# Kernel optimization log

Measured on AMD Instinct MI355X. Metric: run time of the kernel, lower is better.

Reference implementation:

```python
import jax, jax.numpy as jnp
import numpy as np

N_NODES = 20000
N_EDGES = 160000
N_GRAPHS = 16
NEG_INF = -1e30


def gcn_conv(x, edge_index, edge_weight, W, b):
    # PyG GCNConv with improved=True: add self-loops with weight 2.0,
    # symmetric degree normalization, linear transform, scatter-add aggregation.
    N = x.shape[0]
    row, col = edge_index[0], edge_index[1]
    loop = jnp.arange(N)
    row = jnp.concatenate([row, loop])
    col = jnp.concatenate([col, loop])
    ew = jnp.concatenate([edge_weight, jnp.full((N,), 2.0, edge_weight.dtype)])
    deg = jax.ops.segment_sum(ew, col, num_segments=N)
    dinv = jnp.where(deg > 0, deg ** -0.5, 0.0)  # deg_inv_sqrt, inf -> 0
    norm = dinv[row] * ew * dinv[col]            # [E+N]
    xl = x @ W                                   # [N, out]
    out = jax.ops.segment_sum(xl[row] * norm[:, None], col, num_segments=N)
    return out + b


def segment_softmax_masked(logits, mask, batch, num_segments):
    # softmax over masked entries, grouped by graph id (torch_geometric softmax
    # after masked_select); unmasked-out positions return 0.
    neg = jnp.asarray(NEG_INF, logits.dtype)
    ml = jnp.where(mask, logits, neg)
    mx = jax.ops.segment_max(ml, batch, num_segments=num_segments)
    ex = jnp.where(mask, jnp.exp(logits - mx[batch]), 0.0)
    s = jax.ops.segment_sum(ex, batch, num_segments=num_segments)
    return ex / jnp.maximum(s[batch], 1e-16)


def setup_inputs() -> dict:
    key = jax.random.key(0)
    ks = jax.random.split(key, 12)
    x = jax.random.normal(ks[0], (N_NODES, 5), dtype=jnp.float32)
    edge_index = jax.random.randint(ks[1], (2, N_EDGES), 0, N_NODES)
    edge_weight = jax.random.uniform(ks[2], (N_EDGES,), dtype=jnp.float32)
    mask = jax.random.randint(ks[3], (N_NODES,), 0, 2).astype(bool)
    batch = jnp.sort(jax.random.randint(ks[4], (N_NODES,), 0, N_GRAPHS))
    # parameters (Glorot-ish scaling)
    W1 = jax.random.normal(ks[5], (5, 1000), dtype=jnp.float32) / np.sqrt(5)
    b1 = jnp.zeros((1000,), jnp.float32)
    W2 = jax.random.normal(ks[6], (1000, 1000), dtype=jnp.float32) / np.sqrt(1000)
    b2 = jnp.zeros((1000,), jnp.float32)
    Wf = jax.random.normal(ks[7], (1000, 1), dtype=jnp.float32) / np.sqrt(1000)
    bf = jnp.zeros((1,), jnp.float32)
    return {"x": x, "edge_weight": edge_weight, "W1": W1, "b1": b1,
            "W2": W2, "b2": b2, "Wf": Wf, "bf": bf,
            "edge_index": edge_index, "mask": mask, "batch": batch}


def reference(x, edge_weight, W1, b1, W2, b2, Wf, bf, edge_index, mask, batch):
    h = jax.nn.relu(gcn_conv(x, edge_index, edge_weight, W1, b1))
    h = jax.nn.relu(gcn_conv(h, edge_index, edge_weight, W2, b2))
    # dropout treated as identity (eval mode) for a deterministic reference
    logits = (h @ Wf + bf)[:, 0]  # [N]
    return segment_softmax_masked(logits, mask, batch, N_GRAPHS)
```

## Files before the change

### kernel.cpp

```cpp
#include <hip/hip_runtime.h>

#define NN 20000
#define NE 160000
#define NG 16
#define KP 1024
#define MT2 160
#define MPAD2 (MT2*128)
#define NBLK 79

typedef __attribute__((ext_vector_type(8))) short bf16x8;
typedef __attribute__((ext_vector_type(4))) float f32x4;

#define GAS __attribute__((address_space(1)))
#define LAS __attribute__((address_space(3)))

__device__ __forceinline__ unsigned short f2bf(float f) {
    unsigned int u = __float_as_uint(f);
    u += 0x7FFFu + ((u >> 16) & 1u);
    return (unsigned short)(u >> 16);
}

__device__ __forceinline__ void gld_lds16(const char* g, char* l) {
    __builtin_amdgcn_global_load_lds((GAS void*)g, (LAS void*)l, 16, 0, 0);
}

__global__ void deg_cnt_kernel(const int* __restrict__ ei, const float* __restrict__ ew,
                               float* deg, int* cnt, const void* __restrict__ mask,
                               int* flags) {
    const int e = blockIdx.x * blockDim.x + threadIdx.x;
    if (e < 5000) {
        const unsigned v = ((const unsigned*)mask)[e];
        if (v > 1u) atomicOr(&flags[0], 1);
        if (v != 0u && v != 0x3F800000u) atomicOr(&flags[1], 1);
    }
    if (e >= NE) return;
    const int c = ei[NE + e];
    atomicAdd(&deg[c], ew[e]);
    atomicAdd(&cnt[c], 1);
}

__global__ __launch_bounds__(256) void partial_w2t_kernel(const int* __restrict__ cnt,
        const float* __restrict__ deg, const void* __restrict__ mask,
        const int* __restrict__ flags, int* __restrict__ mtmp,
        float* __restrict__ dinv, int* __restrict__ bcnt, int* __restrict__ bmsk,
        const float* __restrict__ W2, unsigned short* __restrict__ W2t) {
    const int bid = blockIdx.x;
    const int t = threadIdx.x;
    if (bid < NBLK) {
        const int i = bid * 256 + t;
        const int f0 = flags[0], f1 = flags[1];
        int c = 0, mv = 0;
        if (i < NN) {
            c = cnt[i];
            dinv[i] = 1.0f / sqrtf(2.0f + deg[i]);
            if (f0 == 0)      mv = ((const int*)mask)[i] != 0;
            else if (f1 == 0) mv = ((const unsigned*)mask)[i] != 0u;
            else              mv = ((const unsigned char*)mask)[i] != 0;
            mtmp[i] = mv;
        }
        __shared__ int sc[256], sm[256];
        sc[t] = c; sm[t] = mv;
        __syncthreads();
        for (int off = 128; off; off >>= 1) {
            if (t < off) { sc[t] += sc[t + off]; sm[t] += sm[t + off]; }
            __syncthreads();
        }
        if (t == 0) { bcnt[bid] = sc[0]; bmsk[bid] = sm[0]; }
    } else {
        __shared__ float tile[32][33];
        const int bw = bid - NBLK;
        const int n0 = (bw & 31) * 32;
        const int k0 = (bw >> 5) * 32;
        const int tx = t & 31, ty = t >> 5;
#pragma unroll
        for (int j = 0; j < 4; ++j) {
            const int k = k0 + ty + j * 8;
            const int n = n0 + tx;
            tile[ty + j * 8][tx] = (k < 1000 && n < 1000) ? W2[k * 1000 + n] : 0.0f;
        }
        __syncthreads();
#pragma unroll
        for (int j = 0; j < 4; ++j) {
            const int n = n0 + ty + j * 8;
            const int k = k0 + tx;
            W2t[(size_t)n * KP + k] = f2bf(tile[tx][ty + j * 8]);
        }
    }
}

__global__ __launch_bounds__(256) void apply_kernel(const int* __restrict__ cnt,
        const int* __restrict__ mtmp, const int* __restrict__ bcnt,
        const int* __restrict__ bmsk, const int* __restrict__ batch,
        int* __restrict__ offs, int* __restrict__ perm, int* __restrict__ bc,
        int* __restrict__ nm) {
    const int b = blockIdx.x, t = threadIdx.x;
    __shared__ int pbc[128], pbm[128];
    if (t < 128) {
        pbc[t] = (t < NBLK) ? bcnt[t] : 0;
        pbm[t] = (t < NBLK) ? bmsk[t] : 0;
    }
    __syncthreads();
    for (int off = 1; off < 128; off <<= 1) {
        int uc = 0, um = 0;
        if (t < 128 && t >= off) { uc = pbc[t - off]; um = pbm[t - off]; }
        __syncthreads();
        if (t < 128) { pbc[t] += uc; pbm[t] += um; }
        __syncthreads();
    }
    if (b == 0 && t == 0) nm[0] = pbm[NBLK - 1];
    const int bco = (b == 0) ? 0 : pbc[b - 1];
    const int bmo = (b == 0) ? 0 : pbm[b - 1];
    const int i = b * 256 + t;
    const int c  = (i < NN) ? cnt[i]  : 0;
    const int mv = (i < NN) ? mtmp[i] : 0;
    __shared__ int sc[256], sm[256];
    sc[t] = c; sm[t] = mv;
    __syncthreads();
    for (int off = 1; off < 256; off <<= 1) {
        const int uc = (t >= off) ? sc[t - off] : 0;
        const int um = (t >= off) ? sm[t - off] : 0;
        __syncthreads();
        sc[t] += uc; sm[t] += um;
        __syncthreads();
    }
    if (i < NN) {
        offs[i] = bco + sc[t] - c;
        if (mv) {
            const int pos = bmo + sm[t] - 1;
            perm[pos] = i;
            bc[pos] = batch[i];
        }
    }
}

__global__ void scatter_kernel(const int* __restrict__ ei, const float* __restrict__ ew,
                               const float* __restrict__ dinv, const int* __restrict__ offs,
                               int* cursor, int* __restrict__ ssrc, float* __restrict__ snorm) {
    const int e = blockIdx.x * blockDim.x + threadIdx.x;
    if (e >= NE) return;
    const int r = ei[e], c = ei[NE + e];
    const int pos = atomicAdd(&cursor[c], 1);
    const int idx = offs[c] + pos;
    ssrc[idx] = r;
    snorm[idx] = dinv[r] * ew[e] * dinv[c];
}

__global__ __launch_bounds__(256) void axf_kernel(const float* __restrict__ x,
        const int* __restrict__ ssrc, const float* __restrict__ snorm,
        const int* __restrict__ offs, const int* __restrict__ cnt,
        const float* __restrict__ dinv, float* __restrict__ Axf) {
    const int i = blockIdx.x * blockDim.x + threadIdx.x;
    if (i >= NN) return;
    float a0=0,a1=0,a2=0,a3=0,a4=0;
    const int s0 = offs[i], n = cnt[i];
    for (int e = s0; e < s0 + n; ++e) {
        const int r = ssrc[e];
        const float w = snorm[e];
        const float* xr = x + r * 5;
        a0 += w*xr[0]; a1 += w*xr[1]; a2 += w*xr[2]; a3 += w*xr[3]; a4 += w*xr[4];
    }
    const float wl = 2.0f * dinv[i] * dinv[i];
    const float* xi = x + i * 5;
    a0 += wl*xi[0]; a1 += wl*xi[1]; a2 += wl*xi[2]; a3 += wl*xi[3]; a4 += wl*xi[4];
    float* o = Axf + i * 5;
    o[0]=a0; o[1]=a1; o[2]=a2; o[3]=a3; o[4]=a4;
}

__global__ __launch_bounds__(256) void aggW1_kernel(const float* __restrict__ Axf,
        const float* __restrict__ W1, const float* __restrict__ b1,
        const int* __restrict__ ssrc, const float* __restrict__ snorm,
        const int* __restrict__ offs, const int* __restrict__ cnt,
        const float* __restrict__ dinv, const int* __restrict__ perm,
        const int* __restrict__ nm, unsigned short* __restrict__ G) {
    const int t = threadIdx.x;
    __shared__ int s_nm;
    if (t == 0) s_nm = nm[0];
    __syncthreads();
    const int nmv = s_nm;
    const int npad = (nmv + 127) & ~127;
    const int j0 = blockIdx.x * 8;
    if (j0 >= npad) return;

    const bool active = t < 250;
    const int c0 = active ? t * 4 : 1000 + (t - 250) * 4;
    float w[5][4];
    float bb[4];
    if (active) {
#pragma unroll
        for (int f = 0; f < 5; ++f) {
            const float4 wv = *(const float4*)(W1 + f * 1000 + c0);
            w[f][0] = wv.x; w[f][1] = wv.y; w[f][2] = wv.z; w[f][3] = wv.w;
        }
        const float4 b4 = *(const float4*)(b1 + c0);
        bb[0] = b4.x; bb[1] = b4.y; bb[2] = b4.z; bb[3] = b4.w;
    } else {
#pragma unroll
        for (int f = 0; f < 5; ++f) { w[f][0]=0; w[f][1]=0; w[f][2]=0; w[f][3]=0; }
        bb[0]=0; bb[1]=0; bb[2]=0; bb[3]=0;
    }

    __shared__ float4 sax4[64];
    __shared__ float2 sax2[64];
    for (int jj = 0; jj < 8; ++jj) {
        const int j = j0 + jj;
        if (j >= npad) break;
        float acc0 = 0.f, acc1 = 0.f, acc2 = 0.f, acc3 = 0.f;
        if (j < nmv) {
            const int i = perm[j];
            const int s0 = offs[i], n = cnt[i];
            const int total = n + 1;
            for (int base = 0; base < total; base += 64) {
                const int m = (total - base < 64) ? (total - base) : 64;
                __syncthreads();
                if (t < m) {
                    const int idx = base + t;
                    int r; float we;
                    if (idx < n) { r = ssrc[s0 + idx]; we = snorm[s0 + idx]; }
                    else         { r = i; const float dv = dinv[i]; we = 2.0f * dv * dv; }
                    const float* axr = Axf + r * 5;
                    sax4[t] = make_float4(axr[0], axr[1], axr[2], axr[3]);
                    sax2[t] = make_float2(axr[4], we);
                }
                __syncthreads();
#pragma unroll 2
                for (int e = 0; e < m; ++e) {
                    const float4 a4 = sax4[e];
                    const float2 a2 = sax2[e];
                    float z0 = bb[0], z1 = bb[1], z2 = bb[2], z3 = bb[3];
                    z0 += a4.x*w[0][0]; z1 += a4.x*w[0][1]; z2 += a4.x*w[0][2]; z3 += a4.x*w[0][3];
                    z0 += a4.y*w[1][0]; z1 += a4.y*w[1][1]; z2 += a4.y*w[1][2]; z3 += a4.y*w[1][3];
                    z0 += a4.z*w[2][0]; z1 += a4.z*w[2][1]; z2 += a4.z*w[2][2]; z3 += a4.z*w[2][3];
                    z0 += a4.w*w[3][0]; z1 += a4.w*w[3][1]; z2 += a4.w*w[3][2]; z3 += a4.w*w[3][3];
                    z0 += a2.x*w[4][0]; z1 += a2.x*w[4][1]; z2 += a2.x*w[4][2]; z3 += a2.x*w[4][3];
                    const float we = a2.y;
                    acc0 += we * fmaxf(z0, 0.f); acc1 += we * fmaxf(z1, 0.f);
                    acc2 += we * fmaxf(z2, 0.f); acc3 += we * fmaxf(z3, 0.f);
                }
            }
        }
        ushort4 pk;
        pk.x = f2bf(acc0); pk.y = f2bf(acc1); pk.z = f2bf(acc2); pk.w = f2bf(acc3);
        *(ushort4*)(G + (size_t)j * KP + c0) = pk;
    }
}

__global__ __launch_bounds__(256) void gemm_kernel(const unsigned short* __restrict__ A,
                                                   const unsigned short* __restrict__ B,
                                                   const float* __restrict__ b2,
                                                   const float* __restrict__ Wf,
                                                   const int* __restrict__ nm,
                                                   float* __restrict__ logitsC) {
    __shared__ unsigned short As[4096];
    __shared__ unsigned short Bs[4096];
    const int tid = threadIdx.x;
    __shared__ int s_nm;
    if (tid == 0) s_nm = nm[0];
    __syncthreads();
    const int nmv = s_nm;
    const int mstrips = (nmv + 127) >> 7;
    const int bid = blockIdx.x;
    const int tm = (bid >> 6) * 8 + (bid & 7);
    const int tn = (bid >> 3) & 7;
    if (tm >= mstrips) return;
    const int lane = tid & 63;
    const int wv = tid >> 6;
    const int wr = wv >> 1, wc = wv & 1;

    const int chunk = ((tid & 3) ^ ((tid >> 3) & 3)) * 16;
    const int rsub = tid >> 2;
    const char* Ag = (const char*)(A + (size_t)(tm * 128 + rsub) * KP) + chunk;
    const char* Bg = (const char*)(B + (size_t)(tn * 128 + rsub) * KP) + chunk;
    char* AsW = (char*)As + wv * 1024;
    char* BsW = (char*)Bs + wv * 1024;

    f32x4 acc[4][4];
#pragma unroll
    for (int i = 0; i < 4; ++i)
#pragma unroll
        for (int j = 0; j < 4; ++j) acc[i][j] = (f32x4){0.f, 0.f, 0.f, 0.f};

    const int m = lane & 15;
    const int quad = lane >> 4;
    const int sw = quad ^ ((m >> 1) & 3);
    const int aoff = (wr * 64 + m) * 64 + sw * 16;
    const int boff = (wc * 64 + m) * 64 + sw * 16;

    for (int kk = 0; kk < KP; kk += 32) {
        __syncthreads();
        const int kb = kk * 2;
        gld_lds16(Ag + kb,             AsW);
        gld_lds16(Ag + kb + 64 * 2048, AsW + 4096);
        gld_lds16(Bg + kb,             BsW);
        gld_lds16(Bg + kb + 64 * 2048, BsW + 4096);
        __syncthreads();
        bf16x8 af[4], bfv[4];
#pragma unroll
        for (int mt = 0; mt < 4; ++mt)
            af[mt] = *(const bf16x8*)((const char*)As + aoff + mt * 1024);
#pragma unroll
        for (int nt = 0; nt < 4; ++nt)
            bfv[nt] = *(const bf16x8*)((const char*)Bs + boff + nt * 1024);
#pragma unroll
        for (int mt = 0; mt < 4; ++mt)
#pragma unroll
            for (int nt = 0; nt < 4; ++nt)
                acc[mt][nt] = __builtin_amdgcn_mfma_f32_16x16x32_bf16(af[mt], bfv[nt], acc[mt][nt], 0, 0, 0);
    }

    const int col0 = tn * 128 + wc * 64 + m;
    const int row00 = tm * 128 + wr * 64 + quad * 4;
#pragma unroll
    for (int mt = 0; mt < 4; ++mt) {
        float ps0 = 0.f, ps1 = 0.f, ps2 = 0.f, ps3 = 0.f;
#pragma unroll
        for (int nt = 0; nt < 4; ++nt) {
            const int c = col0 + nt * 16;
            const float bbv = (c < 1000) ? b2[c] : 0.0f;
            const float wfv = (c < 1000) ? Wf[c] : 0.0f;
            ps0 += fmaxf(acc[mt][nt][0] + bbv, 0.f) * wfv;
            ps1 += fmaxf(acc[mt][nt][1] + bbv, 0.f) * wfv;
            ps2 += fmaxf(acc[mt][nt][2] + bbv, 0.f) * wfv;
            ps3 += fmaxf(acc[mt][nt][3] + bbv, 0.f) * wfv;
        }
#pragma unroll
        for (int msk = 1; msk < 16; msk <<= 1) {
            ps0 += __shfl_xor(ps0, msk);
            ps1 += __shfl_xor(ps1, msk);
            ps2 += __shfl_xor(ps2, msk);
            ps3 += __shfl_xor(ps3, msk);
        }
        if (m == 0) {
            const int row = row00 + mt * 16;
            if (row + 0 < nmv) atomicAdd(&logitsC[row + 0], ps0);
            if (row + 1 < nmv) atomicAdd(&logitsC[row + 1], ps1);
            if (row + 2 < nmv) atomicAdd(&logitsC[row + 2], ps2);
            if (row + 3 < nmv) atomicAdd(&logitsC[row + 3], ps3);
        }
    }
}

__global__ __launch_bounds__(256) void softmax_kernel(const float* __restrict__ logitsC,
        const int* __restrict__ perm, const int* __restrict__ bc,
        const int* __restrict__ nm, float* __restrict__ out) {
    const int g = blockIdx.x;
    const int t = threadIdx.x;
    __shared__ int s_lo, s_hi;
    __shared__ float red[4];
    __shared__ float sval;
    if (t == 0) {
        const int nmv = nm[0];
        int lo = 0, hi = nmv;
        while (lo < hi) { const int mid = (lo + hi) >> 1; if (bc[mid] < g) lo = mid + 1; else hi = mid; }
        s_lo = lo;
        int lo2 = lo, hi2 = nmv;
        while (lo2 < hi2) { const int mid = (lo2 + hi2) >> 1; if (bc[mid] < g + 1) lo2 = mid + 1; else hi2 = mid; }
        s_hi = lo2;
    }
    __syncthreads();
    const int lo = s_lo, hi = s_hi;
    float mx = -1e30f;
    for (int i = lo + t; i < hi; i += 256) mx = fmaxf(mx, logitsC[i]);
    for (int off = 32; off; off >>= 1) mx = fmaxf(mx, __shfl_down(mx, off));
    if ((t & 63) == 0) red[t >> 6] = mx;
    __syncthreads();
    if (t == 0) sval = fmaxf(fmaxf(red[0], red[1]), fmaxf(red[2], red[3]));
    __syncthreads();
    mx = sval;
    __syncthreads();
    float sm = 0.f;
    for (int i = lo + t; i < hi; i += 256) sm += expf(logitsC[i] - mx);
    for (int off = 32; off; off >>= 1) sm += __shfl_down(sm, off);
    if ((t & 63) == 0) red[t >> 6] = sm;
    __syncthreads();
    if (t == 0) sval = red[0] + red[1] + red[2] + red[3];
    __syncthreads();
    const float inv = 1.0f / fmaxf(sval, 1e-16f);
    for (int i = lo + t; i < hi; i += 256)
        out[perm[i]] = expf(logitsC[i] - mx) * inv;
}

extern "C" void kernel_launch(void* const* d_in, const int* in_sizes, int n_in,
                              void* d_out, int out_size, void* d_ws, size_t ws_size,
                              hipStream_t stream) {
    (void)in_sizes; (void)n_in; (void)ws_size;
    const float* x   = (const float*)d_in[0];
    const float* ew  = (const float*)d_in[1];
    const float* W1  = (const float*)d_in[2];
    const float* b1  = (const float*)d_in[3];
    const float* W2  = (const float*)d_in[4];
    const float* b2  = (const float*)d_in[5];
    const float* Wf  = (const float*)d_in[6];
    const int*   ei  = (const int*)d_in[8];
    const void*  mask  = d_in[9];
    const int*   batch = (const int*)d_in[10];
    float* out = (float*)d_out;

    char* p = (char*)d_ws;
    auto carve = [&](size_t bytes) { char* q = p; p += (bytes + 255) & ~(size_t)255; return q; };
    char* zbase = p;
    float* deg     = (float*)carve(NN * 4);
    int*   cnt     = (int*)carve(NN * 4);
    int*   cursor  = (int*)carve(NN * 4);
    float* logitsC = (float*)carve(MPAD2 * 4);
    int*   flags   = (int*)carve(256);
    size_t zspan = (size_t)(p - zbase);
    int*   offs   = (int*)carve(NN * 4);
    float* dinv   = (float*)carve(NN * 4);
    int*   mtmp   = (int*)carve(NN * 4);
    int*   perm   = (int*)carve(NN * 4);
    int*   bc     = (int*)carve(NN * 4);
    int*   bcnt   = (int*)carve(NBLK * 4);
    int*   bmsk   = (int*)carve(NBLK * 4);
    int*   nmp    = (int*)carve(256);
    int*   ssrc   = (int*)carve(NE * 4);
    float* snorm  = (float*)carve(NE * 4);
    float* Axf    = (float*)carve(NN * 5 * 4);
    unsigned short* W2t = (unsigned short*)carve((size_t)KP * KP * 2);
    unsigned short* G   = (unsigned short*)carve((size_t)MPAD2 * KP * 2);

    hipMemsetAsync(zbase, 0, zspan, stream);
    hipMemsetAsync(out, 0, (size_t)out_size * 4, stream);
    hipLaunchKernelGGL(deg_cnt_kernel,    dim3(625),       dim3(256), 0, stream, ei, ew, deg, cnt, mask, flags);
    hipLaunchKernelGGL(partial_w2t_kernel, dim3(NBLK+1024), dim3(256), 0, stream, cnt, deg, mask, flags, mtmp, dinv, bcnt, bmsk, W2, W2t);
    hipLaunchKernelGGL(apply_kernel,      dim3(NBLK),      dim3(256), 0, stream, cnt, mtmp, bcnt, bmsk, batch, offs, perm, bc, nmp);
    hipLaunchKernelGGL(scatter_kernel,    dim3(625),       dim3(256), 0, stream, ei, ew, dinv, offs, cursor, ssrc, snorm);
    hipLaunchKernelGGL(axf_kernel,        dim3(79),        dim3(256), 0, stream, x, ssrc, snorm, offs, cnt, dinv, Axf);
    hipLaunchKernelGGL(aggW1_kernel,      dim3(MPAD2/8),   dim3(256), 0, stream, Axf, W1, b1, ssrc, snorm, offs, cnt, dinv, perm, nmp, G);
    hipLaunchKernelGGL(gemm_kernel,       dim3(MT2*8),     dim3(256), 0, stream, G, W2t, b2, Wf, nmp, logitsC);
    hipLaunchKernelGGL(softmax_kernel,    dim3(NG),        dim3(256), 0, stream, logitsC, perm, bc, nmp, out);
}
```

Before: 200.1 us.

## Restructure aggW1 to wave-per-row shuffles and fold memsets into kernels

```diff
diff --git a/kernel.cpp b/kernel.cpp
--- a/kernel.cpp
+++ b/kernel.cpp
@@ -43,7 +43,8 @@
         const float* __restrict__ deg, const void* __restrict__ mask,
         const int* __restrict__ flags, int* __restrict__ mtmp,
         float* __restrict__ dinv, int* __restrict__ bcnt, int* __restrict__ bmsk,
-        const float* __restrict__ W2, unsigned short* __restrict__ W2t) {
+        const float* __restrict__ W2, unsigned short* __restrict__ W2t,
+        float* __restrict__ logitsC) {
     const int bid = blockIdx.x;
     const int t = threadIdx.x;
     if (bid < NBLK) {
@@ -69,6 +70,7 @@
     } else {
         __shared__ float tile[32][33];
         const int bw = bid - NBLK;
+        if (t < 20) logitsC[bw * 20 + t] = 0.0f;
         const int n0 = (bw & 31) * 32;
         const int k0 = (bw >> 5) * 32;
         const int tx = t & 31, ty = t >> 5;
@@ -92,7 +94,7 @@
         const int* __restrict__ mtmp, const int* __restrict__ bcnt,
         const int* __restrict__ bmsk, const int* __restrict__ batch,
         int* __restrict__ offs, int* __restrict__ perm, int* __restrict__ bc,
-        int* __restrict__ nm) {
+        int* __restrict__ nm, int* __restrict__ cursor, float* __restrict__ out) {
     const int b = blockIdx.x, t = threadIdx.x;
     __shared__ int pbc[128], pbm[128];
     if (t < 128) {
@@ -124,6 +126,8 @@
         __syncthreads();
     }
     if (i < NN) {
+        cursor[i] = 0;
+        out[i] = 0.0f;
         offs[i] = bco + sc[t] - c;
         if (mv) {
             const int pos = bmo + sm[t] - 1;
@@ -172,76 +176,71 @@
         const int* __restrict__ offs, const int* __restrict__ cnt,
         const float* __restrict__ dinv, const int* __restrict__ perm,
         const int* __restrict__ nm, unsigned short* __restrict__ G) {
-    const int t = threadIdx.x;
-    __shared__ int s_nm;
-    if (t == 0) s_nm = nm[0];
-    __syncthreads();
-    const int nmv = s_nm;
+    const int tid = threadIdx.x;
+    const int wv = tid >> 6;
+    const int lane = tid & 63;
+    const int half = wv & 1;
+    const int j = blockIdx.x * 2 + (wv >> 1);
+    const int nmv = nm[0];
     const int npad = (nmv + 127) & ~127;
-    const int j0 = blockIdx.x * 8;
-    if (j0 >= npad) return;
-
-    const bool active = t < 250;
-    const int c0 = active ? t * 4 : 1000 + (t - 250) * 4;
-    float w[5][4];
-    float bb[4];
-    if (active) {
+    if (j >= npad) return;
+
+    const int c0 = half * 512 + lane * 8;
+    float w1r[5][8], bbr[8];
+#pragma unroll
+    for (int q = 0; q < 2; ++q) {
+        const int c = c0 + q * 4;
+        const bool v = (c <= 996);
 #pragma unroll
         for (int f = 0; f < 5; ++f) {
-            const float4 wv = *(const float4*)(W1 + f * 1000 + c0);
-            w[f][0] = wv.x; w[f][1] = wv.y; w[f][2] = wv.z; w[f][3] = wv.w;
-        }
-        const float4 b4 = *(const float4*)(b1 + c0);
-        bb[0] = b4.x; bb[1] = b4.y; bb[2] = b4.z; bb[3] = b4.w;
-    } else {
-#pragma unroll
-        for (int f = 0; f < 5; ++f) { w[f][0]=0; w[f][1]=0; w[f][2]=0; w[f][3]=0; }
-        bb[0]=0; bb[1]=0; bb[2]=0; bb[3]=0;
-    }
-
-    __shared__ float4 sax4[64];
-    __shared__ float2 sax2[64];
-    for (int jj = 0; jj < 8; ++jj) {
-        const int j = j0 + jj;
-        if (j >= npad) break;
-        float acc0 = 0.f, acc1 = 0.f, acc2 = 0.f, acc3 = 0.f;
-        if (j < nmv) {
-            const int i = perm[j];
-            const int s0 = offs[i], n = cnt[i];
-            const int total = n + 1;
-            for (int base = 0; base < total; base += 64) {
-                const int m = (total - base < 64) ? (total - base) : 64;
-                __syncthreads();
-                if (t < m) {
-                    const int idx = base + t;
-                    int r; float we;
-                    if (idx < n) { r = ssrc[s0 + idx]; we = snorm[s0 + idx]; }
-                    else         { r = i; const float dv = dinv[i]; we = 2.0f * dv * dv; }
-                    const float* axr = Axf + r * 5;
-                    sax4[t] = make_float4(axr[0], axr[1], axr[2], axr[3]);
-                    sax2[t] = make_float2(axr[4], we);
-                }
-                __syncthreads();
+            const float4 w4 = v ? *(const float4*)(W1 + f * 1000 + c)
+                                : make_float4(0.f, 0.f, 0.f, 0.f);
+            w1r[f][q*4+0] = w4.x; w1r[f][q*4+1] = w4.y;
+            w1r[f][q*4+2] = w4.z; w1r[f][q*4+3] = w4.w;
+        }
+        const float4 b4 = v ? *(const float4*)(b1 + c) : make_float4(0.f, 0.f, 0.f, 0.f);
+        bbr[q*4+0] = b4.x; bbr[q*4+1] = b4.y; bbr[q*4+2] = b4.z; bbr[q*4+3] = b4.w;
+    }
+    float acc[8];
+#pragma unroll
+    for (int k = 0; k < 8; ++k) acc[k] = 0.f;
+
+    if (j < nmv) {
+        const int i = perm[j];
+        const int s0 = offs[i], n = cnt[i];
+        const int total = n + 1;
+        for (int base = 0; base < total; base += 64) {
+            const int m = (total - base < 64) ? (total - base) : 64;
+            float a0=0.f, a1=0.f, a2=0.f, a3=0.f, a4=0.f, we=0.f;
+            if (lane < m) {
+                const int idx = base + lane;
+                int r;
+                if (idx < n) { r = ssrc[s0 + idx]; we = snorm[s0 + idx]; }
+                else         { r = i; const float dv = dinv[i]; we = 2.0f * dv * dv; }
+                const float* axr = Axf + r * 5;
+                a0 = axr[0]; a1 = axr[1]; a2 = axr[2]; a3 = axr[3]; a4 = axr[4];
+            }
 #pragma unroll 2
-                for (int e = 0; e < m; ++e) {
-                    const float4 a4 = sax4[e];
-                    const float2 a2 = sax2[e];
-                    float z0 = bb[0], z1 = bb[1], z2 = bb[2], z3 = bb[3];
-                    z0 += a4.x*w[0][0]; z1 += a4.x*w[0][1]; z2 += a4.x*w[0][2]; z3 += a4.x*w[0][3];
-                    z0 += a4.y*w[1][0]; z1 += a4.y*w[1][1]; z2 += a4.y*w[1][2]; z3 += a4.y*w[1][3];
-                    z0 += a4.z*w[2][0]; z1 += a4.z*w[2][1]; z2 += a4.z*w[2][2]; z3 += a4.z*w[2][3];
-                    z0 += a4.w*w[3][0]; z1 += a4.w*w[3][1]; z2 += a4.w*w[3][2]; z3 += a4.w*w[3][3];
-                    z0 += a2.x*w[4][0]; z1 += a2.x*w[4][1]; z2 += a2.x*w[4][2]; z3 += a2.x*w[4][3];
-                    const float we = a2.y;
-                    acc0 += we * fmaxf(z0, 0.f); acc1 += we * fmaxf(z1, 0.f);
-                    acc2 += we * fmaxf(z2, 0.f); acc3 += we * fmaxf(z3, 0.f);
+            for (int e = 0; e < m; ++e) {
+                const float s0v = __shfl(a0, e);
+                const float s1v = __shfl(a1, e);
+                const float s2v = __shfl(a2, e);
+                const float s3v = __shfl(a3, e);
+                const float s4v = __shfl(a4, e);
+                const float swv = __shfl(we, e);
+#pragma unroll
+                for (int k = 0; k < 8; ++k) {
+                    const float z = bbr[k] + s0v * w1r[0][k] + s1v * w1r[1][k]
+                                  + s2v * w1r[2][k] + s3v * w1r[3][k] + s4v * w1r[4][k];
+                    acc[k] += swv * fmaxf(z, 0.f);
                 }
             }
         }
-        ushort4 pk;
-        pk.x = f2bf(acc0); pk.y = f2bf(acc1); pk.z = f2bf(acc2); pk.w = f2bf(acc3);
-        *(ushort4*)(G + (size_t)j * KP + c0) = pk;
-    }
+    }
+    bf16x8 pk;
+#pragma unroll
+    for (int k = 0; k < 8; ++k) pk[k] = (short)f2bf(acc[k]);
+    *(bf16x8*)(G + (size_t)j * KP + c0) = pk;
 }
 
 __global__ __launch_bounds__(256) void gemm_kernel(const unsigned short* __restrict__ A,
@@ -382,7 +381,7 @@
 extern "C" void kernel_launch(void* const* d_in, const int* in_sizes, int n_in,
                               void* d_out, int out_size, void* d_ws, size_t ws_size,
                               hipStream_t stream) {
-    (void)in_sizes; (void)n_in; (void)ws_size;
+    (void)in_sizes; (void)n_in; (void)out_size; (void)ws_size;
     const float* x   = (const float*)d_in[0];
     const float* ew  = (const float*)d_in[1];
     const float* W1  = (const float*)d_in[2];
@@ -400,10 +399,10 @@
     char* zbase = p;
     float* deg     = (float*)carve(NN * 4);
     int*   cnt     = (int*)carve(NN * 4);
+    int*   flags   = (int*)carve(256);
+    size_t zspan = (size_t)(p - zbase);
     int*   cursor  = (int*)carve(NN * 4);
     float* logitsC = (float*)carve(MPAD2 * 4);
-    int*   flags   = (int*)carve(256);
-    size_t zspan = (size_t)(p - zbase);
     int*   offs   = (int*)carve(NN * 4);
     float* dinv   = (float*)carve(NN * 4);
     int*   mtmp   = (int*)carve(NN * 4);
@@ -419,13 +418,12 @@
     unsigned short* G   = (unsigned short*)carve((size_t)MPAD2 * KP * 2);
 
     hipMemsetAsync(zbase, 0, zspan, stream);
-    hipMemsetAsync(out, 0, (size_t)out_size * 4, stream);
-    hipLaunchKernelGGL(deg_cnt_kernel,    dim3(625),       dim3(256), 0, stream, ei, ew, deg, cnt, mask, flags);
-    hipLaunchKernelGGL(partial_w2t_kernel, dim3(NBLK+1024), dim3(256), 0, stream, cnt, deg, mask, flags, mtmp, dinv, bcnt, bmsk, W2, W2t);
-    hipLaunchKernelGGL(apply_kernel,      dim3(NBLK),      dim3(256), 0, stream, cnt, mtmp, bcnt, bmsk, batch, offs, perm, bc, nmp);
-    hipLaunchKernelGGL(scatter_kernel,    dim3(625),       dim3(256), 0, stream, ei, ew, dinv, offs, cursor, ssrc, snorm);
-    hipLaunchKernelGGL(axf_kernel,        dim3(79),        dim3(256), 0, stream, x, ssrc, snorm, offs, cnt, dinv, Axf);
-    hipLaunchKernelGGL(aggW1_kernel,      dim3(MPAD2/8),   dim3(256), 0, stream, Axf, W1, b1, ssrc, snorm, offs, cnt, dinv, perm, nmp, G);
-    hipLaunchKernelGGL(gemm_kernel,       dim3(MT2*8),     dim3(256), 0, stream, G, W2t, b2, Wf, nmp, logitsC);
-    hipLaunchKernelGGL(softmax_kernel,    dim3(NG),        dim3(256), 0, stream, logitsC, perm, bc, nmp, out);
-}
+    hipLaunchKernelGGL(deg_cnt_kernel,     dim3(625),       dim3(256), 0, stream, ei, ew, deg, cnt, mask, flags);
+    hipLaunchKernelGGL(partial_w2t_kernel, dim3(NBLK+1024), dim3(256), 0, stream, cnt, deg, mask, flags, mtmp, dinv, bcnt, bmsk, W2, W2t, logitsC);
+    hipLaunchKernelGGL(apply_kernel,       dim3(NBLK),      dim3(256), 0, stream, cnt, mtmp, bcnt, bmsk, batch, offs, perm, bc, nmp, cursor, out);
+    hipLaunchKernelGGL(scatter_kernel,     dim3(625),       dim3(256), 0, stream, ei, ew, dinv, offs, cursor, ssrc, snorm);
+    hipLaunchKernelGGL(axf_kernel,         dim3(79),        dim3(256), 0, stream, x, ssrc, snorm, offs, cnt, dinv, Axf);
+    hipLaunchKernelGGL(aggW1_kernel,       dim3(MPAD2/2),   dim3(256), 0, stream, Axf, W1, b1, ssrc, snorm, offs, cnt, dinv, perm, nmp, G);
+    hipLaunchKernelGGL(gemm_kernel,        dim3(MT2*8),     dim3(256), 0, stream, G, W2t, b2, Wf, nmp, logitsC);
+    hipLaunchKernelGGL(softmax_kernel,     dim3(NG),        dim3(256), 0, stream, logitsC, perm, bc, nmp, out);
+}
```

Result: no change. 198.5 us (-0.8%).
